# Kernel tuning notes

Hardware: AMD Instinct MI355X
Metric: run time of the kernel (lower is better)

Reference implementation:

```python
import jax, jax.numpy as jnp
import numpy as np


def _gru(xg, W_hh, b_hh):
    # xg: [B, T, 3H] precomputed input-gate projections (x @ W_ih.T + b_ih)
    B, T, H3 = xg.shape
    H = H3 // 3
    h0 = jnp.zeros((B, H), dtype=xg.dtype)

    def step(h, xg_t):
        gh = h @ W_hh.T + b_hh                     # [B, 3H]
        xr, xz, xn = jnp.split(xg_t, 3, axis=-1)   # pytorch gate order: r, z, n
        hr, hz, hn = jnp.split(gh, 3, axis=-1)
        r = jax.nn.sigmoid(xr + hr)
        z = jax.nn.sigmoid(xz + hz)
        n = jnp.tanh(xn + r * hn)
        h_new = (1.0 - z) * n + z * h
        return h_new, h_new

    _, hs = jax.lax.scan(step, h0, jnp.swapaxes(xg, 0, 1))  # hs: [T, B, H]
    return jnp.swapaxes(hs, 0, 1)                            # [B, T, H]


def setup_inputs() -> dict:
    key = jax.random.key(0)
    ks = jax.random.split(key, 11)
    B, T, I, H, O = 32, 512, 512, 1024, 360
    s = lambda k, shape, fan: jax.random.normal(k, shape, jnp.float32) * (1.0 / np.sqrt(fan))
    return {
        "x": jax.random.normal(ks[0], (B, T, I), jnp.float32),
        "W1": s(ks[1], (H, I), I),
        "b1": s(ks[2], (H,), I),
        "W2": s(ks[3], (H, H), H),
        "b2": s(ks[4], (H,), H),
        "W_ih": s(ks[5], (3 * H, H), H),
        "b_ih": s(ks[6], (3 * H,), H),
        "W_hh": s(ks[7], (3 * H, H), H),
        "b_hh": s(ks[8], (3 * H,), H),
        "W_out": s(ks[9], (O, H), H),
        "b_out": s(ks[10], (O,), H),
    }


def reference(x, W1, b1, W2, b2, W_ih, b_ih, W_hh, b_hh, W_out, b_out):
    # blocks: Linear -> ReLU -> Linear -> ReLU
    h = jax.nn.relu(x @ W1.T + b1)        # [B, T, H]
    h = jax.nn.relu(h @ W2.T + b2)        # [B, T, H]
    # GRU: precompute input projections for all timesteps, scan hidden recurrence
    xg = h @ W_ih.T + b_ih                # [B, T, 3H]
    h = _gru(xg, W_hh, b_hh)              # [B, T, H]
    # output projection
    return h @ W_out.T + b_out            # [B, T, O]
```

## Files before the change

kernel.cpp:

```cpp
#include <hip/hip_runtime.h>
#include <hip/hip_bf16.h>

#define B_  32
#define T_  512
#define I_  512
#define H_  1024
#define O_  360
#define H3_ 3072
#define M_  (B_*T_)

static constexpr int GRU_NB = 64;

typedef __bf16 bf16x8 __attribute__((ext_vector_type(8)));
typedef float  f32x4  __attribute__((ext_vector_type(4)));

__device__ __forceinline__ float sigmoidf_(float x) {
  return 1.0f / (1.0f + __expf(-x));
}
__device__ __forceinline__ float ld_f32(const float* p) { return *p; }
__device__ __forceinline__ float ld_f32(const __hip_bfloat16* p) { return __bfloat162float(*p); }
__device__ __forceinline__ void st_f32(float* p, float v) { *p = v; }
__device__ __forceinline__ void st_f32(__hip_bfloat16* p, float v) { *p = __float2bfloat16(v); }
__device__ __forceinline__ unsigned short bf16_bits(float f) {
  __hip_bfloat16 b = __float2bfloat16(f);
  return *reinterpret_cast<unsigned short*>(&b);
}
__device__ __forceinline__ unsigned short bits_of(__hip_bfloat16 b) {
  return *reinterpret_cast<unsigned short*>(&b);
}

__global__ void f32_to_bf16_k(const float* __restrict__ in,
                              __hip_bfloat16* __restrict__ out, int n) {
  int i = blockIdx.x * blockDim.x + threadIdx.x;
  int stride = gridDim.x * blockDim.x;
  for (; i < n; i += stride) out[i] = __float2bfloat16(in[i]);
}

__global__ void gru_init_k(__hip_bfloat16* __restrict__ hbuf,
                           unsigned* __restrict__ tags) {
  const int tid0  = blockIdx.x * blockDim.x + threadIdx.x;
  const int stride = gridDim.x * blockDim.x;
  for (int i = tid0; i < 2 * B_ * H_; i += stride) hbuf[i] = __float2bfloat16(0.0f);
  if (tid0 < 2048) tags[tid0] = 0u;
}

template <int ACT, typename OT>
__global__ __launch_bounds__(256)
void mgemm_bt(const float* __restrict__ A, const float* __restrict__ W,
              const float* __restrict__ bias, OT* __restrict__ C,
              int M, int N, int K, int lda) {
  __shared__ __hip_bfloat16 Ah[128][40], Al[128][40];
  __shared__ __hip_bfloat16 Wh[128][40], Wl[128][40];
  const int tid  = threadIdx.x;
  const int lane = tid & 63;
  const int wv   = tid >> 6;
  const int bm   = blockIdx.y * 128;
  const int bn   = blockIdx.x * 128;
  const int msub = (wv & 1) * 64;
  const int nsub = (wv >> 1) * 64;
  const int fr   = lane & 15;
  const int fk   = lane >> 4;

  f32x4 acc[4][4];
#pragma unroll
  for (int i = 0; i < 4; ++i)
#pragma unroll
    for (int j = 0; j < 4; ++j) acc[i][j] = (f32x4){0.f, 0.f, 0.f, 0.f};

  const int sr = tid >> 1;
  const int sc = (tid & 1) * 16;
  const float* Ap = A + (size_t)(bm + sr) * lda + sc;
  const bool wok = (bn + sr) < N;
  const float* Wp = W + (size_t)(wok ? (bn + sr) : 0) * K + sc;

  for (int k0 = 0; k0 < K; k0 += 32) {
    float av[16], wvv[16];
#pragma unroll
    for (int j = 0; j < 4; ++j) {
      float4 t = *(const float4*)(Ap + k0 + j * 4);
      av[j*4+0] = t.x; av[j*4+1] = t.y; av[j*4+2] = t.z; av[j*4+3] = t.w;
      float4 u = wok ? *(const float4*)(Wp + k0 + j * 4)
                     : make_float4(0.f, 0.f, 0.f, 0.f);
      wvv[j*4+0] = u.x; wvv[j*4+1] = u.y; wvv[j*4+2] = u.z; wvv[j*4+3] = u.w;
    }

    unsigned pah[8], pal[8], pwh[8], pwl[8];
#pragma unroll
    for (int e = 0; e < 8; ++e) {
      __hip_bfloat16 a0 = __float2bfloat16(av[2*e]);
      __hip_bfloat16 a1 = __float2bfloat16(av[2*e+1]);
      pah[e] = (unsigned)bits_of(a0) | ((unsigned)bits_of(a1) << 16);
      pal[e] = (unsigned)bf16_bits(av[2*e]   - __bfloat162float(a0)) |
               ((unsigned)bf16_bits(av[2*e+1] - __bfloat162float(a1)) << 16);
      __hip_bfloat16 w0 = __float2bfloat16(wvv[2*e]);
      __hip_bfloat16 w1 = __float2bfloat16(wvv[2*e+1]);
      pwh[e] = (unsigned)bits_of(w0) | ((unsigned)bits_of(w1) << 16);
      pwl[e] = (unsigned)bf16_bits(wvv[2*e]   - __bfloat162float(w0)) |
               ((unsigned)bf16_bits(wvv[2*e+1] - __bfloat162float(w1)) << 16);
    }

    __syncthreads();
    *(uint4*)&Ah[sr][sc]     = make_uint4(pah[0], pah[1], pah[2], pah[3]);
    *(uint4*)&Ah[sr][sc + 8] = make_uint4(pah[4], pah[5], pah[6], pah[7]);
    *(uint4*)&Al[sr][sc]     = make_uint4(pal[0], pal[1], pal[2], pal[3]);
    *(uint4*)&Al[sr][sc + 8] = make_uint4(pal[4], pal[5], pal[6], pal[7]);
    *(uint4*)&Wh[sr][sc]     = make_uint4(pwh[0], pwh[1], pwh[2], pwh[3]);
    *(uint4*)&Wh[sr][sc + 8] = make_uint4(pwh[4], pwh[5], pwh[6], pwh[7]);
    *(uint4*)&Wl[sr][sc]     = make_uint4(pwl[0], pwl[1], pwl[2], pwl[3]);
    *(uint4*)&Wl[sr][sc + 8] = make_uint4(pwl[4], pwl[5], pwl[6], pwl[7]);
    __syncthreads();

    bf16x8 ah[4], al[4];
#pragma unroll
    for (int mf = 0; mf < 4; ++mf) {
      ah[mf] = *(const bf16x8*)&Ah[msub + mf * 16 + fr][fk * 8];
      al[mf] = *(const bf16x8*)&Al[msub + mf * 16 + fr][fk * 8];
    }
#pragma unroll
    for (int nf = 0; nf < 4; ++nf) {
      bf16x8 bh = *(const bf16x8*)&Wh[nsub + nf * 16 + fr][fk * 8];
      bf16x8 bl = *(const bf16x8*)&Wl[nsub + nf * 16 + fr][fk * 8];
#pragma unroll
      for (int mf = 0; mf < 4; ++mf) {
        acc[mf][nf] = __builtin_amdgcn_mfma_f32_16x16x32_bf16(ah[mf], bh, acc[mf][nf], 0, 0, 0);
        acc[mf][nf] = __builtin_amdgcn_mfma_f32_16x16x32_bf16(ah[mf], bl, acc[mf][nf], 0, 0, 0);
        acc[mf][nf] = __builtin_amdgcn_mfma_f32_16x16x32_bf16(al[mf], bh, acc[mf][nf], 0, 0, 0);
      }
    }
  }

#pragma unroll
  for (int nf = 0; nf < 4; ++nf) {
    const int n = bn + nsub + nf * 16 + fr;
    if (n < N) {
      const float bj = bias[n];
#pragma unroll
      for (int mf = 0; mf < 4; ++mf)
#pragma unroll
        for (int r = 0; r < 4; ++r) {
          const int m = bm + msub + mf * 16 + fk * 4 + r;
          float v = acc[mf][nf][r] + bj;
          if (ACT) v = fmaxf(v, 0.0f);
          st_f32(&C[(size_t)m * N + n], v);
        }
    }
  }
}

template <typename XT>
__global__ __launch_bounds__(256)
void gru_scan(const XT* xg,
              const __hip_bfloat16* __restrict__ Wbf,
              const float* __restrict__ bhh,
              float* hs, int hs_ld,
              __hip_bfloat16* hbuf,
              unsigned* tags) {
  __shared__ uint4 WL4[6144];
  __shared__ float PS[128 * 13];
  const int tid  = threadIdx.x;
  const int lane = tid & 63;
  const int wv   = tid >> 6;
  const int bt   = wv & 1;
  const int kh   = wv >> 1;
  const int col  = lane & 15;
  const int krow = lane >> 4;
  const int u0   = blockIdx.x * 16;
  const int u    = u0 + col;
  const int bb   = bt * 16 + krow * 4;
  const int c7   = col & 7;

  for (int idx = tid; idx < 6144; idx += 256) {
    const int g = idx >> 11;
    const int l = (idx >> 7) & 15;
    const int c = idx & 127;
    const uint4 src = *(const uint4*)(Wbf + ((size_t)(g * H_ + u0 + l)) * H_ + c * 8);
    WL4[g * 2048 + l * 128 + (c ^ (l & 7))] = src;
  }
  __syncthreads();

  const float bhr = bhh[u];
  const float bhz = bhh[H_ + u];
  const float bhn = bhh[2 * H_ + u];

  const unsigned* mytag = tags + (((lane << 1) | bt) << 4);
  unsigned* ourtag = tags + (((blockIdx.x << 1) | bt) << 4);

  float* psme = PS + (bt * 64 + lane) * 13;

  f32x4 hold = {0.f, 0.f, 0.f, 0.f};

  float pxr[4], pxz[4], pxn[4];
  if (kh == 0) {
#pragma unroll
    for (int c = 0; c < 4; ++c) {
      const XT* xp = xg + ((size_t)(bb + c) * T_ + 0) * H3_;
      pxr[c] = ld_f32(xp + u);
      pxz[c] = ld_f32(xp + H_ + u);
      pxn[c] = ld_f32(xp + 2 * H_ + u);
    }
  }

  for (int t = 0; t < T_; ++t) {
    const int cur = t & 1;

    if (t > 0) {
      for (;;) {
        unsigned tg = __hip_atomic_load(mytag, __ATOMIC_RELAXED,
                                        __HIP_MEMORY_SCOPE_AGENT);
        if (!__any(tg < (unsigned)t)) break;
        __builtin_amdgcn_s_sleep(1);
      }
      __builtin_amdgcn_sched_barrier(0);
    }

    int tz;
    asm volatile("v_mov_b32 %0, 0" : "=v"(tz));
    const uint4* WLp = WL4 + col * 128 + tz;

    const unsigned long long* ab =
        (const unsigned long long*)(hbuf + cur * (B_ * H_)) +
        (size_t)(bt * 16 + col) * 256 + kh * 128 + krow * 2;

    f32x4 ar = {0.f, 0.f, 0.f, 0.f};
    f32x4 az = {0.f, 0.f, 0.f, 0.f};
    f32x4 an = {0.f, 0.f, 0.f, 0.f};
#pragma unroll 16
    for (int ks = 0; ks < 16; ++ks) {
      union { unsigned long long q[2]; bf16x8 v; } A;
      A.q[0] = __hip_atomic_load(ab + ks * 8 + 0, __ATOMIC_RELAXED, __HIP_MEMORY_SCOPE_AGENT);
      A.q[1] = __hip_atomic_load(ab + ks * 8 + 1, __ATOMIC_RELAXED, __HIP_MEMORY_SCOPE_AGENT);
      const int cx = (krow + (kh * 16 + ks) * 4) ^ c7;
      bf16x8 wrv = __builtin_bit_cast(bf16x8, WLp[cx]);
      bf16x8 wzv = __builtin_bit_cast(bf16x8, WLp[2048 + cx]);
      bf16x8 wnv = __builtin_bit_cast(bf16x8, WLp[4096 + cx]);
      ar = __builtin_amdgcn_mfma_f32_16x16x32_bf16(A.v, wrv, ar, 0, 0, 0);
      az = __builtin_amdgcn_mfma_f32_16x16x32_bf16(A.v, wzv, az, 0, 0, 0);
      an = __builtin_amdgcn_mfma_f32_16x16x32_bf16(A.v, wnv, an, 0, 0, 0);
    }

    if (kh == 1) {
#pragma unroll
      for (int c = 0; c < 4; ++c) {
        psme[c]     = ar[c];
        psme[4 + c] = az[c];
        psme[8 + c] = an[c];
      }
    }
    __syncthreads();

    if (kh == 0) {
#pragma unroll
      for (int c = 0; c < 4; ++c) {
        ar[c] += psme[c];
        az[c] += psme[4 + c];
        an[c] += psme[8 + c];
      }

      float hv[4];
#pragma unroll
      for (int c = 0; c < 4; ++c) {
        const float r = sigmoidf_(pxr[c] + ar[c] + bhr);
        const float z = sigmoidf_(pxz[c] + az[c] + bhz);
        const float n = tanhf(pxn[c] + r * (an[c] + bhn));
        const float h = (1.0f - z) * n + z * hold[c];
        hold[c] = h;
        hv[c] = h;
      }

      unsigned* hn32 = (unsigned*)(hbuf + (cur ^ 1) * (B_ * H_));
      const int ue2 = (u & ~1) >> 1;
      const int c0 = (lane & 1) ? 2 : 0;
#pragma unroll
      for (int c = 0; c < 4; ++c) {
        const float other = __shfl_xor(hv[c], 1, 64);
        unsigned p;
        if (lane & 1)
          p = (unsigned)bf16_bits(other) | ((unsigned)bf16_bits(hv[c]) << 16);
        else
          p = (unsigned)bf16_bits(hv[c]) | ((unsigned)bf16_bits(other) << 16);
        if (c == c0 || c == c0 + 1)
          __hip_atomic_store(hn32 + (size_t)(bb + c) * 512 + ue2, p,
                             __ATOMIC_RELAXED, __HIP_MEMORY_SCOPE_AGENT);
      }

      asm volatile("s_waitcnt vmcnt(0)" ::: "memory");
      if (lane == 0)
        __hip_atomic_store(ourtag, (unsigned)(t + 1),
                           __ATOMIC_RELAXED, __HIP_MEMORY_SCOPE_AGENT);

#pragma unroll
      for (int c = 0; c < 4; ++c)
        hs[((size_t)(bb + c) * T_ + t) * hs_ld + u] = hv[c];

      if (t + 1 < T_) {
#pragma unroll
        for (int c = 0; c < 4; ++c) {
          const XT* xp = xg + ((size_t)(bb + c) * T_ + (t + 1)) * H3_;
          pxr[c] = ld_f32(xp + u);
          pxz[c] = ld_f32(xp + H_ + u);
          pxn[c] = ld_f32(xp + 2 * H_ + u);
        }
      }
    }
  }
}

extern "C" void kernel_launch(void* const* d_in, const int* in_sizes, int n_in,
                              void* d_out, int out_size, void* d_ws, size_t ws_size,
                              hipStream_t stream) {
  const float* x    = (const float*)d_in[0];
  const float* W1   = (const float*)d_in[1];
  const float* b1   = (const float*)d_in[2];
  const float* W2   = (const float*)d_in[3];
  const float* b2   = (const float*)d_in[4];
  const float* Wih  = (const float*)d_in[5];
  const float* bih  = (const float*)d_in[6];
  const float* Whh  = (const float*)d_in[7];
  const float* bhh  = (const float*)d_in[8];
  const float* Wout = (const float*)d_in[9];
  const float* bout = (const float*)d_in[10];
  float* out = (float*)d_out;

  const size_t MB = (size_t)1 << 20;
  char* ws = (char*)d_ws;

  if (ws_size >= 256 * MB) {
    float* h2 = (float*)ws;
    float* h1 = (float*)(ws + 64 * MB);
    float* xg = (float*)(ws + 64 * MB);
    __hip_bfloat16* Wbf  = (__hip_bfloat16*)ws;
    __hip_bfloat16* hbuf = (__hip_bfloat16*)(ws + 8 * MB);
    unsigned* tags = (unsigned*)(ws + 9 * MB);
    float* hs = xg;  const int hs_ld = H3_;

    mgemm_bt<1, float><<<dim3(8, 128), 256, 0, stream>>>(x, W1, b1, h1, M_, H_, I_, I_);
    mgemm_bt<1, float><<<dim3(8, 128), 256, 0, stream>>>(h1, W2, b2, h2, M_, H_, H_, H_);
    mgemm_bt<0, float><<<dim3(24, 128), 256, 0, stream>>>(h2, Wih, bih, xg, M_, H3_, H_, H_);
    f32_to_bf16_k<<<768, 256, 0, stream>>>(Whh, Wbf, H3_ * H_);
    gru_init_k<<<32, 256, 0, stream>>>(hbuf, tags);
    gru_scan<float><<<GRU_NB, 256, 0, stream>>>(xg, Wbf, bhh, hs, hs_ld, hbuf, tags);
    mgemm_bt<0, float><<<dim3(3, 128), 256, 0, stream>>>(hs, Wout, bout, out, M_, O_, H_, hs_ld);
  } else if (ws_size >= 167 * MB) {
    float* h2 = (float*)ws;
    float* hs = (float*)ws;
    float* h1 = (float*)(ws + 64 * MB);
    __hip_bfloat16* xg   = (__hip_bfloat16*)(ws + 64 * MB);
    __hip_bfloat16* Wbf  = (__hip_bfloat16*)(ws + 160 * MB);
    __hip_bfloat16* hbuf = (__hip_bfloat16*)(ws + 166 * MB);
    unsigned* tags = (unsigned*)(ws + 166 * MB + 256 * 1024);

    mgemm_bt<1, float><<<dim3(8, 128), 256, 0, stream>>>(x, W1, b1, h1, M_, H_, I_, I_);
    mgemm_bt<1, float><<<dim3(8, 128), 256, 0, stream>>>(h1, W2, b2, h2, M_, H_, H_, H_);
    mgemm_bt<0, __hip_bfloat16><<<dim3(24, 128), 256, 0, stream>>>(h2, Wih, bih, xg, M_, H3_, H_, H_);
    f32_to_bf16_k<<<768, 256, 0, stream>>>(Whh, Wbf, H3_ * H_);
    gru_init_k<<<32, 256, 0, stream>>>(hbuf, tags);
    gru_scan<__hip_bfloat16><<<GRU_NB, 256, 0, stream>>>(xg, Wbf, bhh, hs, H_, hbuf, tags);
    mgemm_bt<0, float><<<dim3(3, 128), 256, 0, stream>>>(hs, Wout, bout, out, M_, O_, H_, H_);
  }
}
```

Baseline: 4.527 ms.

## Split GRU gate epilogue across both K-half waves with per-wave tags

The GRU recurrent kernel now has both K-split waves exchange half of their partial sums through LDS. Each wave then finishes the gate math for two of its four batch rows, instead of one wave doing all four while the other idles. Each wave publishes its own progress tag, so consumers poll two tags per producer. A cheaper exp-based tanh replaces tanhf. The intent is to shorten the serial per-step critical path, at the cost of doubled tag polling traffic and slightly reduced tanh accuracy.

```diff
diff --git a/kernel.cpp b/kernel.cpp
--- a/kernel.cpp
+++ b/kernel.cpp
@@ -17,6 +17,10 @@
 __device__ __forceinline__ float sigmoidf_(float x) {
   return 1.0f / (1.0f + __expf(-x));
 }
+__device__ __forceinline__ float tanhf_(float x) {
+  float e = __expf(2.0f * x);
+  return 1.0f - 2.0f / (e + 1.0f);
+}
 __device__ __forceinline__ float ld_f32(const float* p) { return *p; }
 __device__ __forceinline__ float ld_f32(const __hip_bfloat16* p) { return __bfloat162float(*p); }
 __device__ __forceinline__ void st_f32(float* p, float v) { *p = v; }
@@ -41,7 +45,7 @@
   const int tid0  = blockIdx.x * blockDim.x + threadIdx.x;
   const int stride = gridDim.x * blockDim.x;
   for (int i = tid0; i < 2 * B_ * H_; i += stride) hbuf[i] = __float2bfloat16(0.0f);
-  if (tid0 < 2048) tags[tid0] = 0u;
+  if (tid0 < 4096) tags[tid0] = 0u;
 }
 
 template <int ACT, typename OT>
@@ -168,6 +172,7 @@
   const int u    = u0 + col;
   const int bb   = bt * 16 + krow * 4;
   const int c7   = col & 7;
+  const int cb   = kh * 2;
 
   for (int idx = tid; idx < 6144; idx += 256) {
     const int g = idx >> 11;
@@ -182,32 +187,33 @@
   const float bhz = bhh[H_ + u];
   const float bhn = bhh[2 * H_ + u];
 
-  const unsigned* mytag = tags + (((lane << 1) | bt) << 4);
-  unsigned* ourtag = tags + (((blockIdx.x << 1) | bt) << 4);
+  const unsigned* tp0 = tags + ((((lane << 1) | bt) << 1) << 4);
+  unsigned* ourtag = tags + ((((blockIdx.x << 1) | bt) << 1 | kh) << 4);
 
   float* psme = PS + (bt * 64 + lane) * 13;
 
-  f32x4 hold = {0.f, 0.f, 0.f, 0.f};
-
-  float pxr[4], pxz[4], pxn[4];
-  if (kh == 0) {
-#pragma unroll
-    for (int c = 0; c < 4; ++c) {
-      const XT* xp = xg + ((size_t)(bb + c) * T_ + 0) * H3_;
-      pxr[c] = ld_f32(xp + u);
-      pxz[c] = ld_f32(xp + H_ + u);
-      pxn[c] = ld_f32(xp + 2 * H_ + u);
-    }
+  float hold[2] = {0.f, 0.f};
+
+  float pxr[2], pxz[2], pxn[2];
+#pragma unroll
+  for (int c = 0; c < 2; ++c) {
+    const XT* xp = xg + ((size_t)(bb + cb + c) * T_ + 0) * H3_;
+    pxr[c] = ld_f32(xp + u);
+    pxz[c] = ld_f32(xp + H_ + u);
+    pxn[c] = ld_f32(xp + 2 * H_ + u);
   }
 
   for (int t = 0; t < T_; ++t) {
     const int cur = t & 1;
 
     if (t > 0) {
+      const unsigned want = (unsigned)t;
       for (;;) {
-        unsigned tg = __hip_atomic_load(mytag, __ATOMIC_RELAXED,
-                                        __HIP_MEMORY_SCOPE_AGENT);
-        if (!__any(tg < (unsigned)t)) break;
+        const unsigned g0 = __hip_atomic_load(tp0, __ATOMIC_RELAXED,
+                                              __HIP_MEMORY_SCOPE_AGENT);
+        const unsigned g1 = __hip_atomic_load(tp0 + 16, __ATOMIC_RELAXED,
+                                              __HIP_MEMORY_SCOPE_AGENT);
+        if (!__any((g0 < want) || (g1 < want))) break;
         __builtin_amdgcn_s_sleep(1);
       }
       __builtin_amdgcn_sched_barrier(0);
@@ -238,68 +244,59 @@
       an = __builtin_amdgcn_mfma_f32_16x16x32_bf16(A.v, wnv, an, 0, 0, 0);
     }
 
-    if (kh == 1) {
-#pragma unroll
-      for (int c = 0; c < 4; ++c) {
-        psme[c]     = ar[c];
-        psme[4 + c] = az[c];
-        psme[8 + c] = an[c];
+    {
+      const int co = 2 - cb;
+      const int wbase = kh ? 6 : 0;
+      psme[wbase + 0] = ar[co];     psme[wbase + 1] = az[co];
+      psme[wbase + 2] = an[co];     psme[wbase + 3] = ar[co + 1];
+      psme[wbase + 4] = az[co + 1]; psme[wbase + 5] = an[co + 1];
+    }
+    __syncthreads();
+
+    const int rbase = kh ? 0 : 6;
+    float hv[2];
+#pragma unroll
+    for (int c = 0; c < 2; ++c) {
+      const float sr_ = ar[cb + c] + psme[rbase + c * 3 + 0];
+      const float sz_ = az[cb + c] + psme[rbase + c * 3 + 1];
+      const float sn_ = an[cb + c] + psme[rbase + c * 3 + 2];
+      const float r = sigmoidf_(pxr[c] + sr_ + bhr);
+      const float z = sigmoidf_(pxz[c] + sz_ + bhz);
+      const float n = tanhf_(pxn[c] + r * (sn_ + bhn));
+      const float h = (1.0f - z) * n + z * hold[c];
+      hold[c] = h;
+      hv[c] = h;
+    }
+
+    unsigned* hn32 = (unsigned*)(hbuf + (cur ^ 1) * (B_ * H_));
+    const int ue2 = (u & ~1) >> 1;
+#pragma unroll
+    for (int c = 0; c < 2; ++c) {
+      const float other = __shfl_xor(hv[c], 1, 64);
+      if (!(lane & 1)) {
+        const unsigned p = (unsigned)bf16_bits(hv[c]) |
+                           ((unsigned)bf16_bits(other) << 16);
+        __hip_atomic_store(hn32 + (size_t)(bb + cb + c) * 512 + ue2, p,
+                           __ATOMIC_RELAXED, __HIP_MEMORY_SCOPE_AGENT);
       }
     }
-    __syncthreads();
-
-    if (kh == 0) {
-#pragma unroll
-      for (int c = 0; c < 4; ++c) {
-        ar[c] += psme[c];
-        az[c] += psme[4 + c];
-        an[c] += psme[8 + c];
-      }
-
-      float hv[4];
-#pragma unroll
-      for (int c = 0; c < 4; ++c) {
-        const float r = sigmoidf_(pxr[c] + ar[c] + bhr);
-        const float z = sigmoidf_(pxz[c] + az[c] + bhz);
-        const float n = tanhf(pxn[c] + r * (an[c] + bhn));
-        const float h = (1.0f - z) * n + z * hold[c];
-        hold[c] = h;
-        hv[c] = h;
-      }
-
-      unsigned* hn32 = (unsigned*)(hbuf + (cur ^ 1) * (B_ * H_));
-      const int ue2 = (u & ~1) >> 1;
-      const int c0 = (lane & 1) ? 2 : 0;
-#pragma unroll
-      for (int c = 0; c < 4; ++c) {
-        const float other = __shfl_xor(hv[c], 1, 64);
-        unsigned p;
-        if (lane & 1)
-          p = (unsigned)bf16_bits(other) | ((unsigned)bf16_bits(hv[c]) << 16);
-        else
-          p = (unsigned)bf16_bits(hv[c]) | ((unsigned)bf16_bits(other) << 16);
-        if (c == c0 || c == c0 + 1)
-          __hip_atomic_store(hn32 + (size_t)(bb + c) * 512 + ue2, p,
-                             __ATOMIC_RELAXED, __HIP_MEMORY_SCOPE_AGENT);
-      }
-
-      asm volatile("s_waitcnt vmcnt(0)" ::: "memory");
-      if (lane == 0)
-        __hip_atomic_store(ourtag, (unsigned)(t + 1),
-                           __ATOMIC_RELAXED, __HIP_MEMORY_SCOPE_AGENT);
-
-#pragma unroll
-      for (int c = 0; c < 4; ++c)
-        hs[((size_t)(bb + c) * T_ + t) * hs_ld + u] = hv[c];
-
-      if (t + 1 < T_) {
-#pragma unroll
-        for (int c = 0; c < 4; ++c) {
-          const XT* xp = xg + ((size_t)(bb + c) * T_ + (t + 1)) * H3_;
-          pxr[c] = ld_f32(xp + u);
-          pxz[c] = ld_f32(xp + H_ + u);
-          pxn[c] = ld_f32(xp + 2 * H_ + u);
-        }
+
+    asm volatile("s_waitcnt vmcnt(0)" ::: "memory");
+    if (lane == 0)
+      __hip_atomic_store(ourtag, (unsigned)(t + 1),
+                         __ATOMIC_RELAXED, __HIP_MEMORY_SCOPE_AGENT);
+
+#pragma unroll
+    for (int c = 0; c < 2; ++c)
+      hs[((size_t)(bb + cb + c) * T_ + t) * hs_ld + u] = hv[c];
+
+    if (t + 1 < T_) {
+#pragma unroll
+      for (int c = 0; c < 2; ++c) {
+        const XT* xp = xg + ((size_t)(bb + cb + c) * T_ + (t + 1)) * H3_;
+        pxr[c] = ld_f32(xp + u);
+        pxz[c] = ld_f32(xp + H_ + u);
+        pxn[c] = ld_f32(xp + 2 * H_ + u);
       }
     }
   }
```

After: 3.771 ms. 1.2x faster.
